# Performance work log

Hardware: AMD Instinct MI355X
Metric: run time of the kernel (lower is better)

## Reference

```python
import jax, jax.numpy as jnp
import numpy as np

E = 512      # embed_dim
H = 8        # num_heads
HD = E // H  # head_dim
TGT = 512
SRC = 2048
B = 16


def setup_inputs() -> dict:
    key = jax.random.key(0)
    ks = jax.random.split(key, 10)
    inp = {
        "query": jax.random.normal(ks[0], (TGT, B, E), dtype=jnp.float32),
        "key": jax.random.normal(ks[1], (SRC, B, E), dtype=jnp.float32),
        "value": jax.random.normal(ks[2], (SRC, B, E), dtype=jnp.float32),
        "in_proj_weight": jax.random.normal(ks[3], (3 * E, E), dtype=jnp.float32) * 0.02,
        "in_proj_bias": jax.random.normal(ks[4], (3 * E,), dtype=jnp.float32) * 0.02,
        "bias_k": jax.random.normal(ks[5], (1, 1, E), dtype=jnp.float32) * 0.02,
        "bias_v": jax.random.normal(ks[6], (1, 1, E), dtype=jnp.float32) * 0.02,
        "out_proj_weight": jax.random.normal(ks[7], (E, E), dtype=jnp.float32) * 0.02,
        "out_proj_bias": jnp.zeros((E,), dtype=jnp.float32),
        "key_padding_mask": jax.random.randint(ks[8], (B, SRC), 0, 2).astype(bool),
    }
    return inp


def reference(query, key, value, in_proj_weight, in_proj_bias, bias_k, bias_v,
              out_proj_weight, out_proj_bias, key_padding_mask):
    tgt_len, bsz, embed_dim = query.shape
    scaling = float(HD) ** -0.5

    # manual in-projection (query != key, key is value -> separate q, fused kv)
    q = query @ in_proj_weight[:E].T + in_proj_bias[:E]
    k = key @ in_proj_weight[E:2 * E].T + in_proj_bias[E:2 * E]
    v = value @ in_proj_weight[2 * E:].T + in_proj_bias[2 * E:]
    q = q * scaling

    # bias_k / bias_v concatenation along src dim; pad key_padding_mask with False
    k = jnp.concatenate([k, jnp.broadcast_to(bias_k, (1, bsz, E))], axis=0)
    v = jnp.concatenate([v, jnp.broadcast_to(bias_v, (1, bsz, E))], axis=0)
    kpm = jnp.pad(key_padding_mask, ((0, 0), (0, 1)))  # [B, SRC+1]

    src_len = k.shape[0]
    # [len, B, E] -> [B*H, len, HD]
    q = q.reshape(tgt_len, bsz * H, HD).transpose(1, 0, 2)
    k = k.reshape(src_len, bsz * H, HD).transpose(1, 0, 2)
    v = v.reshape(src_len, bsz * H, HD).transpose(1, 0, 2)

    scores = jnp.einsum('bth,bsh->bts', q, k)  # [B*H, TGT, SRC+1]
    mask = kpm[:, None, None, :]               # [B, 1, 1, SRC+1]
    scores = scores.reshape(bsz, H, tgt_len, src_len)
    scores = jnp.where(mask, -jnp.inf, scores).reshape(bsz * H, tgt_len, src_len)
    attn = jax.nn.softmax(scores, axis=-1)

    out = jnp.einsum('bts,bsh->bth', attn, v)                 # [B*H, TGT, HD]
    out = out.transpose(1, 0, 2).reshape(tgt_len, bsz, E)     # [TGT, B, E]
    out = out @ out_proj_weight.T + out_proj_bias
    return out, attn
```

## Files before the change

kernel.cpp:

```cpp
#include <hip/hip_runtime.h>
#include <hip/hip_bf16.h>

#define E    512
#define H    8
#define HD   64
#define TGT  512
#define SRC  2048
#define S1   2049
#define S1P  2112
#define NB   16
#define BH   128
#define NCH  33
#define PW   2120

typedef __attribute__((ext_vector_type(8))) short short8;
typedef __attribute__((ext_vector_type(4))) float floatx4;

__device__ __forceinline__ unsigned short f2bf(float x) {
    unsigned u = __float_as_uint(x);
    u = (u + 0x7FFF + ((u >> 16) & 1)) >> 16;
    return (unsigned short)u;
}

__device__ __forceinline__ unsigned short f2bf1(float x) {
    __hip_bfloat16 h = __float2bfloat16(x);
    return *(unsigned short*)&h;
}

__device__ __forceinline__ int4 cvt8(const float4 f0, const float4 f1) {
    __hip_bfloat162 o[4];
    o[0] = __float22bfloat162_rn({f0.x, f0.y});
    o[1] = __float22bfloat162_rn({f0.z, f0.w});
    o[2] = __float22bfloat162_rn({f1.x, f1.y});
    o[3] = __float22bfloat162_rn({f1.z, f1.w});
    return *(int4*)o;
}

__global__ __launch_bounds__(256) void cvt_bf16(const float* __restrict__ src,
    unsigned short* __restrict__ dst, const int n8)
{
    const int i = blockIdx.x * 256 + threadIdx.x;
    if (i >= n8) return;
    const float4 f0 = ((const float4*)src)[(size_t)i * 2];
    const float4 f1 = ((const float4*)src)[(size_t)i * 2 + 1];
    ((int4*)dst)[i] = cvt8(f0, f1);
}

__global__ __launch_bounds__(256) void proj_all(
    const unsigned short* __restrict__ q_bf, const unsigned short* __restrict__ k_bf,
    const unsigned short* __restrict__ v_bf, const unsigned short* __restrict__ wi,
    const float* __restrict__ ipb,
    unsigned short* __restrict__ qbh, unsigned short* __restrict__ kbuf,
    unsigned short* __restrict__ vtbuf)
{
    const int z = blockIdx.z;
    if (z == 0 && blockIdx.y >= 64) return;
    __shared__ __align__(16) unsigned short As[128][72];
    __shared__ __align__(16) unsigned short Bs[64][72];
    const unsigned short* X = (z == 0) ? q_bf : (z == 1) ? k_bf : v_bf;
    const unsigned short* W = wi + (size_t)z * 262144;
    const float* bias = ipb + z * E;
    const int tid  = threadIdx.x;
    const int c0   = blockIdx.x << 6;
    const int r0   = blockIdx.y << 7;
    const int w    = tid >> 6, lane = tid & 63, c = lane & 15, quad = lane >> 4;
    floatx4 acc[2][4] = {};
    for (int k0 = 0; k0 < E; k0 += 64) {
#pragma unroll
        for (int i = 0; i < 4; ++i) {
            const int idx = tid + (i << 8);
            const int r = idx >> 3, q = (idx & 7) << 3;
            *(int4*)&As[r][q] = *(const int4*)&X[(size_t)(r0 + r) * E + k0 + q];
        }
#pragma unroll
        for (int i = 0; i < 2; ++i) {
            const int idx = tid + (i << 8);
            const int r = idx >> 3, q = (idx & 7) << 3;
            *(int4*)&Bs[r][q] = *(const int4*)&W[(size_t)(c0 + r) * E + k0 + q];
        }
        __syncthreads();
#pragma unroll
        for (int kh = 0; kh < 2; ++kh) {
            short8 a0 = *(const short8*)&As[(w << 5) + c][(kh << 5) + (quad << 3)];
            short8 a1 = *(const short8*)&As[(w << 5) + 16 + c][(kh << 5) + (quad << 3)];
#pragma unroll
            for (int n = 0; n < 4; ++n) {
                short8 b = *(const short8*)&Bs[(n << 4) + c][(kh << 5) + (quad << 3)];
                acc[0][n] = __builtin_amdgcn_mfma_f32_16x16x32_bf16(a0, b, acc[0][n], 0, 0, 0);
                acc[1][n] = __builtin_amdgcn_mfma_f32_16x16x32_bf16(a1, b, acc[1][n], 0, 0, 0);
            }
        }
        __syncthreads();
    }
    if (z == 2) {
        const int h = c0 >> 6;
#pragma unroll
        for (int mt = 0; mt < 2; ++mt) {
#pragma unroll
            for (int reg = 0; reg < 4; ++reg) {
                const int local = (w << 5) + (mt << 4) + (quad << 2) + reg;
#pragma unroll
                for (int n = 0; n < 4; ++n) {
                    const int hd = (n << 4) + c;
                    As[local][hd] = f2bf1(acc[mt][n][reg] + bias[c0 + hd]);
                }
            }
        }
        __syncthreads();
        const int s0v = blockIdx.y << 3;
#pragma unroll
        for (int i = 0; i < 4; ++i) {
            const int idx = tid + (i << 8);
            const int b = idx & 15, hd = idx >> 4;
            unsigned short tmp[8];
#pragma unroll
            for (int j = 0; j < 8; ++j) tmp[j] = As[(j << 4) + b][hd];
            *(int4*)&vtbuf[((size_t)(b * H + h) * HD + hd) * S1P + s0v] = *(int4*)tmp;
        }
        return;
    }
    unsigned short* Y = (z == 0) ? qbh : kbuf;
    const int ld = (z == 0) ? TGT : S1P;
    const float scale = (z == 0) ? 0.125f : 1.0f;
#pragma unroll
    for (int mt = 0; mt < 2; ++mt) {
#pragma unroll
        for (int reg = 0; reg < 4; ++reg) {
            const int rg = r0 + (w << 5) + (mt << 4) + (quad << 2) + reg;
            const int t = rg >> 4, b = rg & 15;
#pragma unroll
            for (int n = 0; n < 4; ++n) {
                const int col = c0 + (n << 4) + c;
                const int h = col >> 6, hd = col & 63;
                const float v = (acc[mt][n][reg] + bias[col]) * scale;
                Y[((size_t)(b * H + h) * ld + t) * HD + hd] = f2bf1(v);
            }
        }
    }
}

#define FB_BIAS  8192
#define FB_KPAD  64512
#define FB_VPAD  516096
__global__ __launch_bounds__(256) void fill_bias(const float* __restrict__ bk,
    const float* __restrict__ bv,
    unsigned short* __restrict__ kbuf, unsigned short* __restrict__ vtbuf)
{
    const int idx = blockIdx.x * 256 + threadIdx.x;
    if (idx < FB_BIAS) {
        const int bh = idx >> 6, hd = idx & 63, h = bh & 7;
        kbuf[((size_t)bh * S1P + SRC) * HD + hd] = f2bf(bk[h * HD + hd]);
        vtbuf[((size_t)bh * HD + hd) * S1P + SRC] = f2bf(bv[h * HD + hd]);
    } else if (idx < FB_BIAS + FB_KPAD) {
        const int i = idx - FB_BIAS;
        const int bh = i / 504, o = i % 504;
        const int4 z = {0, 0, 0, 0};
        ((int4*)&kbuf[((size_t)bh * S1P + S1) * HD])[o] = z;
    } else if (idx < FB_BIAS + FB_KPAD + FB_VPAD) {
        const int i = idx - FB_BIAS - FB_KPAD;
        const int bh = i / 4032, r = i % 4032;
        const int hd = r / 63, s = S1 + r % 63;
        vtbuf[((size_t)bh * HD + hd) * S1P + s] = 0;
    }
}

__global__ __launch_bounds__(512, 4) void attn_fused(
    const unsigned short* __restrict__ qbh,
    const unsigned short* __restrict__ kbuf,
    const unsigned short* __restrict__ vtbuf,
    const int* __restrict__ kpm,
    float* __restrict__ attn, unsigned short* __restrict__ ctx)
{
    __shared__ __align__(16) unsigned short P[16][PW];
    __shared__ float cpart[16][68];
    __shared__ float sums[8][16];
    __shared__ float linv[16];
    const int tid = threadIdx.x;
    const int t0  = blockIdx.x << 4;
    const int bh  = blockIdx.y;
    const int bb  = bh >> 3;
    const int w = tid >> 6, lane = tid & 63, c = lane & 15, quad = lane >> 4;

    const unsigned short* qr = &qbh[((size_t)bh * TGT + t0 + c) * HD + (quad << 3)];
    short8 qa0 = *(const short8*)qr;
    short8 qa1 = *(const short8*)(qr + 32);

#define LOADK(D0, D1, M, CH) do {                                               \
        const unsigned short* kb_ = &kbuf[((size_t)bh * S1P + ((CH) << 6)) * HD]; \
        _Pragma("unroll")                                                       \
        for (int n_ = 0; n_ < 4; ++n_) {                                        \
            const unsigned short* kr_ = kb_ + ((n_ << 4) + c) * HD + (quad << 3); \
            D0[n_] = *(const short8*)kr_;                                       \
            D1[n_] = *(const short8*)(kr_ + 32);                                \
        }                                                                       \
        _Pragma("unroll")                                                       \
        for (int n_ = 0; n_ < 4; ++n_) {                                        \
            const int s_ = ((CH) << 6) + (n_ << 4) + c;                         \
            M[n_] = (s_ < SRC) ? (kpm[bb * SRC + s_] ? 3e38f : 0.f)             \
                               : ((s_ == SRC) ? 0.f : 3e38f);                   \
        }                                                                       \
    } while (0)

#define PIN(D0, D1) asm volatile("" :                                          \
        "+v"(D0[0]), "+v"(D0[1]), "+v"(D0[2]), "+v"(D0[3]),                     \
        "+v"(D1[0]), "+v"(D1[1]), "+v"(D1[2]), "+v"(D1[3]))

#define QK_COMPUTE(CH, B0, B1, M) do {                                          \
        const int s0_ = (CH) << 6;                                              \
        floatx4 sc_[4] = {};                                                    \
        _Pragma("unroll")                                                       \
        for (int n_ = 0; n_ < 4; ++n_) {                                        \
            sc_[n_] = __builtin_amdgcn_mfma_f32_16x16x32_bf16(qa0, B0[n_], sc_[n_], 0, 0, 0); \
            sc_[n_] = __builtin_amdgcn_mfma_f32_16x16x32_bf16(qa1, B1[n_], sc_[n_], 0, 0, 0); \
        }                                                                       \
        _Pragma("unroll")                                                       \
        for (int n_ = 0; n_ < 4; ++n_) {                                        \
            _Pragma("unroll")                                                   \
            for (int rg_ = 0; rg_ < 4; ++rg_) {                                 \
                const float p_ = __expf(sc_[n_][rg_] - M[n_]);                  \
                rs[rg_] += p_;                                                  \
                P[(quad << 2) + rg_][s0_ + (n_ << 4) + c] = f2bf1(p_);          \
            }                                                                   \
        }                                                                       \
    } while (0)

    float rs[4] = {0.f, 0.f, 0.f, 0.f};
    short8 kb0[4], kb1[4];
    float mk[4];
    LOADK(kb0, kb1, mk, w);
    int ch;
    for (ch = w; ch + 8 < NCH; ch += 8) {
        short8 nb0[4], nb1[4];
        float nm[4];
        LOADK(nb0, nb1, nm, ch + 8);
        PIN(nb0, nb1);
        QK_COMPUTE(ch, kb0, kb1, mk);
#pragma unroll
        for (int n = 0; n < 4; ++n) { kb0[n] = nb0[n]; kb1[n] = nb1[n]; mk[n] = nm[n]; }
    }
    QK_COMPUTE(ch, kb0, kb1, mk);

#pragma unroll
    for (int reg = 0; reg < 4; ++reg) {
        float v = rs[reg];
        v += __shfl_xor(v, 1); v += __shfl_xor(v, 2);
        v += __shfl_xor(v, 4); v += __shfl_xor(v, 8);
        rs[reg] = v;
    }
    if (c == 0) {
#pragma unroll
        for (int reg = 0; reg < 4; ++reg)
            sums[w][(quad << 2) + reg] = rs[reg];
    }
    __syncthreads();
    if (tid < 16) {
        float s = 0.f;
#pragma unroll
        for (int i = 0; i < 8; ++i) s += sums[i][tid];
        linv[tid] = 1.0f / s;
    }
    __syncthreads();

    const int hs = w & 3, kh2 = w >> 2;
    const int base = kh2 * 1056;
    const unsigned short* vrow = &vtbuf[((size_t)bh * HD + (hs << 4) + c) * S1P + base];
#define LV(U) (*(const short8*)&vrow[((U) << 5) + (quad << 3)])
#define LP(U) (*(const short8*)&P[c][base + ((U) << 5) + (quad << 3)])
    floatx4 ca0 = {}, ca1 = {};
    short8 vt = LV(32);
    short8 v0 = LV(0), v1 = LV(1), v2 = LV(2), v3 = LV(3);
#pragma unroll
    for (int u = 0; u < 32; u += 4) {
        ca0 = __builtin_amdgcn_mfma_f32_16x16x32_bf16(LP(u),     v0, ca0, 0, 0, 0);
        ca1 = __builtin_amdgcn_mfma_f32_16x16x32_bf16(LP(u + 1), v1, ca1, 0, 0, 0);
        if (u < 28) { v0 = LV(u + 4); v1 = LV(u + 5); }
        ca0 = __builtin_amdgcn_mfma_f32_16x16x32_bf16(LP(u + 2), v2, ca0, 0, 0, 0);
        ca1 = __builtin_amdgcn_mfma_f32_16x16x32_bf16(LP(u + 3), v3, ca1, 0, 0, 0);
        if (u < 28) { v2 = LV(u + 6); v3 = LV(u + 7); }
    }
    ca0 = __builtin_amdgcn_mfma_f32_16x16x32_bf16(LP(32), vt, ca0, 0, 0, 0);
    if (kh2 == 1) {
#pragma unroll
        for (int reg = 0; reg < 4; ++reg)
            cpart[(quad << 2) + reg][(hs << 4) + c] = ca0[reg] + ca1[reg];
    }
    __syncthreads();
    if (kh2 == 0) {
#pragma unroll
        for (int reg = 0; reg < 4; ++reg) {
            const int row = (quad << 2) + reg;
            const float v = (ca0[reg] + ca1[reg] + cpart[row][(hs << 4) + c]) * linv[row];
            ctx[((size_t)bh * TGT + t0 + row) * HD + (hs << 4) + c] = f2bf1(v);
        }
    }

    for (int p = w; p < 16; p += 8) {
        const int s0 = p << 7;
#pragma unroll
        for (int r = 0; r < 16; ++r) {
            const unsigned pk = *(const unsigned*)&P[r][s0 + (lane << 1)];
            const float li = linv[r];
            const size_t a = ((size_t)bh * TGT + t0 + r) * S1 + s0 + (lane << 1);
            attn[a]     = __uint_as_float((pk & 0xFFFFu) << 16) * li;
            attn[a + 1] = __uint_as_float(pk & 0xFFFF0000u) * li;
        }
    }
    if (w == 7 && lane < 16) {
        const float p = __uint_as_float((unsigned)P[lane][2048] << 16) * linv[lane];
        attn[((size_t)bh * TGT + t0 + lane) * S1 + 2048] = p;
    }
#undef LOADK
#undef PIN
#undef QK_COMPUTE
#undef LV
#undef LP
}

__global__ __launch_bounds__(256) void outproj_gemm(const unsigned short* __restrict__ ctx,
    const unsigned short* __restrict__ W, const float* __restrict__ bias,
    float* __restrict__ out)
{
    __shared__ __align__(16) unsigned short As[128][72];
    __shared__ __align__(16) unsigned short Bs[64][72];
    const int tid = threadIdx.x;
    const int c0  = blockIdx.x << 6;
    const int r0  = blockIdx.y << 7;
    const int w   = tid >> 6, lane = tid & 63, c = lane & 15, quad = lane >> 4;
    floatx4 acc[2][4] = {};
    for (int k0 = 0; k0 < E; k0 += 64) {
        const int h = k0 >> 6;
#pragma unroll
        for (int i = 0; i < 4; ++i) {
            const int idx = tid + (i << 8);
            const int r = idx >> 3, q = (idx & 7) << 3;
            const int rg = r0 + r, t = rg >> 4, b = rg & 15;
            *(int4*)&As[r][q] = *(const int4*)&ctx[((size_t)(b * H + h) * TGT + t) * HD + q];
        }
#pragma unroll
        for (int i = 0; i < 2; ++i) {
            const int idx = tid + (i << 8);
            const int r = idx >> 3, q = (idx & 7) << 3;
            *(int4*)&Bs[r][q] = *(const int4*)&W[(size_t)(c0 + r) * E + k0 + q];
        }
        __syncthreads();
#pragma unroll
        for (int kh = 0; kh < 2; ++kh) {
            short8 a0 = *(const short8*)&As[(w << 5) + c][(kh << 5) + (quad << 3)];
            short8 a1 = *(const short8*)&As[(w << 5) + 16 + c][(kh << 5) + (quad << 3)];
#pragma unroll
            for (int n = 0; n < 4; ++n) {
                short8 b = *(const short8*)&Bs[(n << 4) + c][(kh << 5) + (quad << 3)];
                acc[0][n] = __builtin_amdgcn_mfma_f32_16x16x32_bf16(a0, b, acc[0][n], 0, 0, 0);
                acc[1][n] = __builtin_amdgcn_mfma_f32_16x16x32_bf16(a1, b, acc[1][n], 0, 0, 0);
            }
        }
        __syncthreads();
    }
#pragma unroll
    for (int mt = 0; mt < 2; ++mt) {
#pragma unroll
        for (int reg = 0; reg < 4; ++reg) {
            const int rg = r0 + (w << 5) + (mt << 4) + (quad << 2) + reg;
#pragma unroll
            for (int n = 0; n < 4; ++n) {
                const int col = c0 + (n << 4) + c;
                out[(size_t)rg * E + col] = acc[mt][n][reg] + bias[col];
            }
        }
    }
}

extern "C" void kernel_launch(void* const* d_in, const int* in_sizes, int n_in,
                              void* d_out, int out_size, void* d_ws, size_t ws_size,
                              hipStream_t stream)
{
    const float* query  = (const float*)d_in[0];
    const float* key    = (const float*)d_in[1];
    const float* value  = (const float*)d_in[2];
    const float* ipw    = (const float*)d_in[3];
    const float* ipb    = (const float*)d_in[4];
    const float* bias_k = (const float*)d_in[5];
    const float* bias_v = (const float*)d_in[6];
    const float* opw    = (const float*)d_in[7];
    const float* opb    = (const float*)d_in[8];
    const int*   kpm    = (const int*)d_in[9];

    float* out  = (float*)d_out;
    float* attn = out + (size_t)TGT * NB * E;

    unsigned short* k_bf = (unsigned short*)attn;
    unsigned short* v_bf = k_bf + (size_t)16777216;

    char* ws = (char*)d_ws;
    unsigned short* q_bf  = (unsigned short*)ws;
    unsigned short* wi_bf = q_bf  + (size_t)4194304;
    unsigned short* wo_bf = wi_bf + (size_t)786432;
    unsigned short* qbh   = wo_bf + (size_t)262144;
    unsigned short* kbuf  = qbh   + (size_t)4194304;
    unsigned short* vtbuf = kbuf  + (size_t)17301504;
    unsigned short* ctx   = vtbuf + (size_t)17301504;

    cvt_bf16<<<dim3(2048), 256, 0, stream>>>(query, q_bf, 524288);
    cvt_bf16<<<dim3(8192), 256, 0, stream>>>(key,   k_bf, 2097152);
    cvt_bf16<<<dim3(8192), 256, 0, stream>>>(value, v_bf, 2097152);
    cvt_bf16<<<dim3(384),  256, 0, stream>>>(ipw,   wi_bf, 98304);
    cvt_bf16<<<dim3(128),  256, 0, stream>>>(opw,   wo_bf, 32768);

    proj_all<<<dim3(8, 256, 3), 256, 0, stream>>>(q_bf, k_bf, v_bf, wi_bf, ipb,
                                                  qbh, kbuf, vtbuf);

    fill_bias<<<dim3(2300), 256, 0, stream>>>(bias_k, bias_v, kbuf, vtbuf);

    attn_fused<<<dim3(32, 128), 512, 0, stream>>>(qbh, kbuf, vtbuf, kpm, attn, ctx);
    outproj_gemm<<<dim3(8, 64), 256, 0, stream>>>(ctx, wo_bf, opb, out);
}
```

Measured before the change: 1.025 ms.

## Process 32 query rows per block with 16 waves to reuse K loads

The attention block now covers 32 target rows with 1024 threads instead of 16 rows with 512. Each wave loads a K chunk once and runs QK MFMAs for two 16-row query tiles, halving K global traffic per output row. The software prefetch of the next K chunk is removed because each wave now handles only two or three chunks. The P tile in LDS doubles to about 135KB, so occupancy drops to one block per CU, and the larger 1024-thread block may limit latency hiding.

```diff
diff --git a/kernel.cpp b/kernel.cpp
--- a/kernel.cpp
+++ b/kernel.cpp
@@ -164,19 +164,19 @@
     }
 }
 
-__global__ __launch_bounds__(512, 4) void attn_fused(
+__global__ __launch_bounds__(1024) void attn_fused(
     const unsigned short* __restrict__ qbh,
     const unsigned short* __restrict__ kbuf,
     const unsigned short* __restrict__ vtbuf,
     const int* __restrict__ kpm,
     float* __restrict__ attn, unsigned short* __restrict__ ctx)
 {
-    __shared__ __align__(16) unsigned short P[16][PW];
-    __shared__ float cpart[16][68];
-    __shared__ float sums[8][16];
-    __shared__ float linv[16];
+    __shared__ __align__(16) unsigned short P[32][PW];
+    __shared__ float cpart[32][68];
+    __shared__ float sums[16][32];
+    __shared__ float linv[32];
     const int tid = threadIdx.x;
-    const int t0  = blockIdx.x << 4;
+    const int t0  = blockIdx.x << 5;
     const int bh  = blockIdx.y;
     const int bb  = bh >> 3;
     const int w = tid >> 6, lane = tid & 63, c = lane & 15, quad = lane >> 4;
@@ -184,88 +184,103 @@
     const unsigned short* qr = &qbh[((size_t)bh * TGT + t0 + c) * HD + (quad << 3)];
     short8 qa0 = *(const short8*)qr;
     short8 qa1 = *(const short8*)(qr + 32);
-
-#define LOADK(D0, D1, M, CH) do {                                               \
+    const unsigned short* qr2 = qr + (size_t)16 * HD;
+    short8 qb0 = *(const short8*)qr2;
+    short8 qb1 = *(const short8*)(qr2 + 32);
+
+#define LOADK(CH) do {                                                          \
         const unsigned short* kb_ = &kbuf[((size_t)bh * S1P + ((CH) << 6)) * HD]; \
         _Pragma("unroll")                                                       \
         for (int n_ = 0; n_ < 4; ++n_) {                                        \
             const unsigned short* kr_ = kb_ + ((n_ << 4) + c) * HD + (quad << 3); \
-            D0[n_] = *(const short8*)kr_;                                       \
-            D1[n_] = *(const short8*)(kr_ + 32);                                \
+            kb0[n_] = *(const short8*)kr_;                                      \
+            kb1[n_] = *(const short8*)(kr_ + 32);                               \
         }                                                                       \
         _Pragma("unroll")                                                       \
         for (int n_ = 0; n_ < 4; ++n_) {                                        \
             const int s_ = ((CH) << 6) + (n_ << 4) + c;                         \
-            M[n_] = (s_ < SRC) ? (kpm[bb * SRC + s_] ? 3e38f : 0.f)             \
-                               : ((s_ == SRC) ? 0.f : 3e38f);                   \
+            mk[n_] = (s_ < SRC) ? (kpm[bb * SRC + s_] ? 3e38f : 0.f)            \
+                                : ((s_ == SRC) ? 0.f : 3e38f);                  \
         }                                                                       \
     } while (0)
 
-#define PIN(D0, D1) asm volatile("" :                                          \
-        "+v"(D0[0]), "+v"(D0[1]), "+v"(D0[2]), "+v"(D0[3]),                     \
-        "+v"(D1[0]), "+v"(D1[1]), "+v"(D1[2]), "+v"(D1[3]))
-
-#define QK_COMPUTE(CH, B0, B1, M) do {                                          \
+#define QK2(CH) do {                                                            \
         const int s0_ = (CH) << 6;                                              \
         floatx4 sc_[4] = {};                                                    \
         _Pragma("unroll")                                                       \
         for (int n_ = 0; n_ < 4; ++n_) {                                        \
-            sc_[n_] = __builtin_amdgcn_mfma_f32_16x16x32_bf16(qa0, B0[n_], sc_[n_], 0, 0, 0); \
-            sc_[n_] = __builtin_amdgcn_mfma_f32_16x16x32_bf16(qa1, B1[n_], sc_[n_], 0, 0, 0); \
+            sc_[n_] = __builtin_amdgcn_mfma_f32_16x16x32_bf16(qa0, kb0[n_], sc_[n_], 0, 0, 0); \
+            sc_[n_] = __builtin_amdgcn_mfma_f32_16x16x32_bf16(qa1, kb1[n_], sc_[n_], 0, 0, 0); \
         }                                                                       \
         _Pragma("unroll")                                                       \
         for (int n_ = 0; n_ < 4; ++n_) {                                        \
             _Pragma("unroll")                                                   \
             for (int rg_ = 0; rg_ < 4; ++rg_) {                                 \
-                const float p_ = __expf(sc_[n_][rg_] - M[n_]);                  \
-                rs[rg_] += p_;                                                  \
+                const float p_ = __expf(sc_[n_][rg_] - mk[n_]);                 \
+                rs0[rg_] += p_;                                                 \
                 P[(quad << 2) + rg_][s0_ + (n_ << 4) + c] = f2bf1(p_);          \
             }                                                                   \
         }                                                                       \
+        floatx4 sd_[4] = {};                                                    \
+        _Pragma("unroll")                                                       \
+        for (int n_ = 0; n_ < 4; ++n_) {                                        \
+            sd_[n_] = __builtin_amdgcn_mfma_f32_16x16x32_bf16(qb0, kb0[n_], sd_[n_], 0, 0, 0); \
+            sd_[n_] = __builtin_amdgcn_mfma_f32_16x16x32_bf16(qb1, kb1[n_], sd_[n_], 0, 0, 0); \
+        }                                                                       \
+        _Pragma("unroll")                                                       \
+        for (int n_ = 0; n_ < 4; ++n_) {                                        \
+            _Pragma("unroll")                                                   \
+            for (int rg_ = 0; rg_ < 4; ++rg_) {                                 \
+                const float p_ = __expf(sd_[n_][rg_] - mk[n_]);                 \
+                rs1[rg_] += p_;                                                 \
+                P[16 + (quad << 2) + rg_][s0_ + (n_ << 4) + c] = f2bf1(p_);     \
+            }                                                                   \
+        }                                                                       \
     } while (0)
 
-    float rs[4] = {0.f, 0.f, 0.f, 0.f};
+    float rs0[4] = {0.f, 0.f, 0.f, 0.f};
+    float rs1[4] = {0.f, 0.f, 0.f, 0.f};
     short8 kb0[4], kb1[4];
     float mk[4];
-    LOADK(kb0, kb1, mk, w);
-    int ch;
-    for (ch = w; ch + 8 < NCH; ch += 8) {
-        short8 nb0[4], nb1[4];
-        float nm[4];
-        LOADK(nb0, nb1, nm, ch + 8);
-        PIN(nb0, nb1);
-        QK_COMPUTE(ch, kb0, kb1, mk);
-#pragma unroll
-        for (int n = 0; n < 4; ++n) { kb0[n] = nb0[n]; kb1[n] = nb1[n]; mk[n] = nm[n]; }
-    }
-    QK_COMPUTE(ch, kb0, kb1, mk);
+    LOADK(w);
+    QK2(w);
+    LOADK(w + 16);
+    QK2(w + 16);
+    if (w == 0) {
+        LOADK(32);
+        QK2(32);
+    }
 
 #pragma unroll
     for (int reg = 0; reg < 4; ++reg) {
-        float v = rs[reg];
-        v += __shfl_xor(v, 1); v += __shfl_xor(v, 2);
-        v += __shfl_xor(v, 4); v += __shfl_xor(v, 8);
-        rs[reg] = v;
+        float v0s = rs0[reg], v1s = rs1[reg];
+        v0s += __shfl_xor(v0s, 1); v0s += __shfl_xor(v0s, 2);
+        v0s += __shfl_xor(v0s, 4); v0s += __shfl_xor(v0s, 8);
+        v1s += __shfl_xor(v1s, 1); v1s += __shfl_xor(v1s, 2);
+        v1s += __shfl_xor(v1s, 4); v1s += __shfl_xor(v1s, 8);
+        rs0[reg] = v0s; rs1[reg] = v1s;
     }
     if (c == 0) {
 #pragma unroll
-        for (int reg = 0; reg < 4; ++reg)
-            sums[w][(quad << 2) + reg] = rs[reg];
+        for (int reg = 0; reg < 4; ++reg) {
+            sums[w][(quad << 2) + reg]      = rs0[reg];
+            sums[w][16 + (quad << 2) + reg] = rs1[reg];
+        }
     }
     __syncthreads();
-    if (tid < 16) {
+    if (tid < 32) {
         float s = 0.f;
 #pragma unroll
-        for (int i = 0; i < 8; ++i) s += sums[i][tid];
+        for (int i = 0; i < 16; ++i) s += sums[i][tid];
         linv[tid] = 1.0f / s;
     }
     __syncthreads();
 
-    const int hs = w & 3, kh2 = w >> 2;
+    const int rh = w >> 3, hs = (w >> 1) & 3, kh2 = w & 1;
     const int base = kh2 * 1056;
     const unsigned short* vrow = &vtbuf[((size_t)bh * HD + (hs << 4) + c) * S1P + base];
 #define LV(U) (*(const short8*)&vrow[((U) << 5) + (quad << 3)])
-#define LP(U) (*(const short8*)&P[c][base + ((U) << 5) + (quad << 3)])
+#define LP(U) (*(const short8*)&P[(rh << 4) + c][base + ((U) << 5) + (quad << 3)])
     floatx4 ca0 = {}, ca1 = {};
     short8 vt = LV(32);
     short8 v0 = LV(0), v1 = LV(1), v2 = LV(2), v3 = LV(3);
@@ -282,22 +297,22 @@
     if (kh2 == 1) {
 #pragma unroll
         for (int reg = 0; reg < 4; ++reg)
-            cpart[(quad << 2) + reg][(hs << 4) + c] = ca0[reg] + ca1[reg];
+            cpart[(rh << 4) + (quad << 2) + reg][(hs << 4) + c] = ca0[reg] + ca1[reg];
     }
     __syncthreads();
     if (kh2 == 0) {
 #pragma unroll
         for (int reg = 0; reg < 4; ++reg) {
-            const int row = (quad << 2) + reg;
+            const int row = (rh << 4) + (quad << 2) + reg;
             const float v = (ca0[reg] + ca1[reg] + cpart[row][(hs << 4) + c]) * linv[row];
             ctx[((size_t)bh * TGT + t0 + row) * HD + (hs << 4) + c] = f2bf1(v);
         }
     }
 
-    for (int p = w; p < 16; p += 8) {
-        const int s0 = p << 7;
-#pragma unroll
-        for (int r = 0; r < 16; ++r) {
+    {
+        const int s0 = w << 7;
+#pragma unroll
+        for (int r = 0; r < 32; ++r) {
             const unsigned pk = *(const unsigned*)&P[r][s0 + (lane << 1)];
             const float li = linv[r];
             const size_t a = ((size_t)bh * TGT + t0 + r) * S1 + s0 + (lane << 1);
@@ -305,13 +320,12 @@
             attn[a + 1] = __uint_as_float(pk & 0xFFFF0000u) * li;
         }
     }
-    if (w == 7 && lane < 16) {
+    if (w == 15 && lane < 32) {
         const float p = __uint_as_float((unsigned)P[lane][2048] << 16) * linv[lane];
         attn[((size_t)bh * TGT + t0 + lane) * S1 + 2048] = p;
     }
 #undef LOADK
-#undef PIN
-#undef QK_COMPUTE
+#undef QK2
 #undef LV
 #undef LP
 }
@@ -411,6 +425,6 @@
 
     fill_bias<<<dim3(2300), 256, 0, stream>>>(bias_k, bias_v, kbuf, vtbuf);
 
-    attn_fused<<<dim3(32, 128), 512, 0, stream>>>(qbh, kbuf, vtbuf, kpm, attn, ctx);
+    attn_fused<<<dim3(16, 128), 1024, 0, stream>>>(qbh, kbuf, vtbuf, kpm, attn, ctx);
     outproj_gemm<<<dim3(8, 64), 256, 0, stream>>>(ctx, wo_bf, opb, out);
 }
```

Result: no change. 1.019 ms (-0.6%).
